# Optimization experiments

Hardware: AMD Instinct MI355X
Metric: run time of the kernel (lower is better)

Reference implementation:

```python
import jax, jax.numpy as jnp
import numpy as np

B, S, D, H, F = 2, 2048, 1024, 16, 4096
DH = D // H
EPS = 1e-6


def layer_norm(x, g, b):
    mu = jnp.mean(x, axis=-1, keepdims=True)
    var = jnp.mean(jnp.square(x - mu), axis=-1, keepdims=True)
    return (x - mu) * jax.lax.rsqrt(var + EPS) * g + b


def setup_inputs() -> dict:
    key = jax.random.key(0)
    ks = jax.random.split(key, 12)
    s_in = 1.0 / np.sqrt(D)
    s_ff = 1.0 / np.sqrt(F)
    return {
        "x_enc": jax.random.normal(ks[0], (B, S, D), jnp.float32),
        "x_pos": jax.random.normal(ks[1], (B, S, D), jnp.float32),
        "wq": jax.random.normal(ks[2], (D, D), jnp.float32) * s_in,
        "bq": jnp.zeros((D,), jnp.float32),
        "wk": jax.random.normal(ks[3], (D, D), jnp.float32) * s_in,
        "bk": jnp.zeros((D,), jnp.float32),
        "wv": jax.random.normal(ks[4], (D, D), jnp.float32) * s_in,
        "bv": jnp.zeros((D,), jnp.float32),
        "wc": jax.random.normal(ks[5], (D, D), jnp.float32) * s_in,
        "bc": jnp.zeros((D,), jnp.float32),
        "w1": jax.random.normal(ks[6], (D, F), jnp.float32) * s_in,
        "b1": jnp.zeros((F,), jnp.float32),
        "w2": jax.random.normal(ks[7], (F, D), jnp.float32) * s_ff,
        "b2": jnp.zeros((D,), jnp.float32),
        "g1": jnp.ones((D,), jnp.float32),
        "be1": jnp.zeros((D,), jnp.float32),
        "g2": jnp.ones((D,), jnp.float32),
        "be2": jnp.zeros((D,), jnp.float32),
    }


def reference(x_enc, x_pos, wq, bq, wk, bk, wv, bv, wc, bc, w1, b1, w2, b2, g1, be1, g2, be2):
    x = x_enc + x_pos  # [B,S,D]

    def split_heads(t):  # [B,S,D] -> [B,H,S,DH]
        return t.reshape(B, S, H, DH).transpose(0, 2, 1, 3)

    q = split_heads(x @ wq + bq)
    k = split_heads(x @ wk + bk)
    v = split_heads(x @ wv + bv)

    scale = jax.lax.rsqrt(jnp.asarray(DH, jnp.float32))
    logits = jnp.einsum("bhqd,bhkd->bhqk", q, k) * scale  # [B,H,S,S]
    weights = jax.nn.softmax(logits, axis=-1)
    attn = jnp.einsum("bhqk,bhkd->bhqd", weights, v)  # [B,H,S,DH]
    attn = attn.transpose(0, 2, 1, 3).reshape(B, S, D)
    attn = attn @ wc + bc

    # residual: x + LN(attn_out)   (dropout inactive in eval)
    a = x + layer_norm(attn, g1, be1)
    ffn = jnp.maximum(a @ w1 + b1, 0.0) @ w2 + b2
    out = a + layer_norm(ffn, g2, be2)
    return out
```

## Files before the change

### kernel.cpp

```cpp
#include <hip/hip_runtime.h>
#include <math.h>

#define B_ 2
#define S_ 2048
#define D_ 1024
#define H_ 16
#define F_ 4096

typedef __bf16 bf16_t;
typedef __bf16 bf16x8 __attribute__((ext_vector_type(8)));
typedef __bf16 bf16x4 __attribute__((ext_vector_type(4)));
typedef float f32x4 __attribute__((ext_vector_type(4)));
typedef float f32x16 __attribute__((ext_vector_type(16)));
typedef _Float16 f16x4 __attribute__((ext_vector_type(4)));
typedef _Float16 f16x8 __attribute__((ext_vector_type(8)));
typedef __fp16 h16x2 __attribute__((ext_vector_type(2)));

__device__ __forceinline__ bf16_t f2b(float f) { return (bf16_t)f; }

__device__ __forceinline__ void gld_lds16(const void* g, void* l) {
  __builtin_amdgcn_global_load_lds(
      (const __attribute__((address_space(1))) unsigned int*)g,
      (__attribute__((address_space(3))) unsigned int*)l, 16, 0, 0);
}

__device__ __forceinline__ void transpose_tile(const float* __restrict__ in,
                                               bf16_t* __restrict__ out,
                                               int K, int N, int bx, int by) {
  __shared__ float tile[64][65];
  int k0 = by * 64, n0 = bx * 64;
  int tid = threadIdx.x;
  int col4 = tid & 15;
  int row = tid >> 4;
#pragma unroll
  for (int rr = 0; rr < 4; ++rr) {
    int r = rr * 16 + row;
    float4 v = *reinterpret_cast<const float4*>(in + (size_t)(k0 + r) * N + n0 + col4 * 4);
    tile[r][col4 * 4 + 0] = v.x;
    tile[r][col4 * 4 + 1] = v.y;
    tile[r][col4 * 4 + 2] = v.z;
    tile[r][col4 * 4 + 3] = v.w;
  }
  __syncthreads();
#pragma unroll
  for (int rr = 0; rr < 4; ++rr) {
    int n = rr * 16 + row;
    bf16x4 o;
    o[0] = f2b(tile[col4 * 4 + 0][n]);
    o[1] = f2b(tile[col4 * 4 + 1][n]);
    o[2] = f2b(tile[col4 * 4 + 2][n]);
    o[3] = f2b(tile[col4 * 4 + 3][n]);
    *reinterpret_cast<bf16x4*>(out + (size_t)(n0 + n) * K + k0 + col4 * 4) = o;
  }
}

__global__ __launch_bounds__(256) void prep_kernel(
    const float* __restrict__ xe, const float* __restrict__ xp,
    bf16_t* __restrict__ XB,
    const float* __restrict__ wq, const float* __restrict__ wk,
    const float* __restrict__ wv, const float* __restrict__ wc,
    const float* __restrict__ w1, const float* __restrict__ w2,
    const float* __restrict__ bq, const float* __restrict__ bk,
    const float* __restrict__ bv,
    bf16_t* __restrict__ Wqkvt, bf16_t* __restrict__ wctb,
    bf16_t* __restrict__ w1tb, bf16_t* __restrict__ w2tb,
    float* __restrict__ bqkv) {
  int bid = blockIdx.x;
  if (bid < 4096) {
    int i = bid * 256 + threadIdx.x;
    float4 av = reinterpret_cast<const float4*>(xe)[i];
    float4 bv4 = reinterpret_cast<const float4*>(xp)[i];
    bf16x4 o;
    o[0] = f2b(av.x + bv4.x); o[1] = f2b(av.y + bv4.y);
    o[2] = f2b(av.z + bv4.z); o[3] = f2b(av.w + bv4.w);
    reinterpret_cast<bf16x4*>(XB)[i] = o;
    return;
  }
  int pb = bid - 4096;
  if (pb < 1024) {
    int seg = pb >> 8, local = pb & 255;
    const float* src = seg == 0 ? wq : (seg == 1 ? wk : (seg == 2 ? wv : wc));
    bf16_t* dst = seg == 3 ? wctb : Wqkvt + (size_t)seg * D_ * D_;
    transpose_tile(src, dst, D_, D_, local & 15, local >> 4);
  } else if (pb < 2048) {
    int local = pb - 1024;
    transpose_tile(w1, w1tb, D_, F_, local & 63, local >> 6);
  } else if (pb < 3072) {
    int local = pb - 2048;
    transpose_tile(w2, w2tb, F_, D_, local & 15, local >> 4);
  } else {
    int i = (pb - 3072) * 256 + threadIdx.x;
    const float* src = i < 1024 ? bq : (i < 2048 ? bk : bv);
    bqkv[i] = src[i & 1023];
  }
}

__global__ __launch_bounds__(256) void gemm_kernel(
    const bf16_t* __restrict__ A, const bf16_t* __restrict__ Bt,
    const float* __restrict__ bias,
    bf16_t* __restrict__ P0, bf16_t* __restrict__ P1,
    bf16_t* __restrict__ P2, bf16_t* __restrict__ P3,
    _Float16* __restrict__ VTout,
    int M, int N, int K, int relu, int kchunk, int rx, int ry) {
  __shared__ bf16_t As[128 * 64];
  __shared__ bf16_t Bs[128 * 64];
  int tid = threadIdx.x;
  int lane = tid & 63, wave = tid >> 6;
  int bx = blockIdx.x, by = blockIdx.y;
  if (rx) {
    int id = by * gridDim.x + bx;
    int j = id & 7, local = id >> 3;
    int regs_x = gridDim.x / rx;
    bx = (j % regs_x) * rx + local % rx;
    by = (j / regs_x) * ry + local / rx;
  }
  int bm = by * 128, bn = bx * 128;
  int wm = (wave >> 1) * 64, wn = (wave & 1) * 64;
  int m32 = lane & 31, khalf = lane >> 5;
  int z = blockIdx.z;
  int kbeg = z * kchunk, kend = kbeg + kchunk;
  f32x16 acc[2][2] = {};

  for (int kt = kbeg; kt < kend; kt += 64) {
    __syncthreads();
#pragma unroll
    for (int c = 0; c < 4; ++c) {
      int e = c * 256 + tid;
      int row = e >> 3, kg = e & 7;
      int kgs = kg ^ (row & 7);
      gld_lds16(A + (size_t)(bm + row) * K + kt + kgs * 8, As + e * 8);
    }
#pragma unroll
    for (int c = 0; c < 4; ++c) {
      int e = c * 256 + tid;
      int row = e >> 3, kg = e & 7;
      int kgs = kg ^ (row & 7);
      gld_lds16(Bt + (size_t)(bn + row) * K + kt + kgs * 8, Bs + e * 8);
    }
    __syncthreads();
#pragma unroll
    for (int kc = 0; kc < 4; ++kc) {
      bf16x8 af[2], bfr[2];
#pragma unroll
      for (int mi = 0; mi < 2; ++mi) {
        int row = wm + mi * 32 + m32;
        int kg = (kc * 2 + khalf) ^ (row & 7);
        af[mi] = *reinterpret_cast<const bf16x8*>(As + row * 64 + kg * 8);
      }
#pragma unroll
      for (int ni = 0; ni < 2; ++ni) {
        int row = wn + ni * 32 + m32;
        int kg = (kc * 2 + khalf) ^ (row & 7);
        bfr[ni] = *reinterpret_cast<const bf16x8*>(Bs + row * 64 + kg * 8);
      }
#pragma unroll
      for (int mi = 0; mi < 2; ++mi)
#pragma unroll
        for (int ni = 0; ni < 2; ++ni)
          acc[mi][ni] = __builtin_amdgcn_mfma_f32_32x32x16_bf16(af[mi], bfr[ni], acc[mi][ni], 0, 0, 0);
    }
  }
  bf16_t* Cb = z == 0 ? P0 : (z == 1 ? P1 : (z == 2 ? P2 : P3));
#pragma unroll
  for (int ni = 0; ni < 2; ++ni) {
    int n = bn + wn + ni * 32 + m32;
    float bz = (bias && z == 0) ? bias[n] : 0.f;
#pragma unroll
    for (int mi = 0; mi < 2; ++mi) {
      float vv[16];
#pragma unroll
      for (int r = 0; r < 16; ++r) {
        float v = acc[mi][ni][r] + bz;
        if (relu) v = fmaxf(v, 0.f);
        vv[r] = v;
      }
      if (VTout && n >= 2048) {
        int h = (n - 2048) >> 6, d = (n - 2048) & 63;
        int bb = bm >> 11;
        _Float16* vtr = VTout + ((size_t)((bb * H_ + h) * 64 + d)) * S_
                        + (bm & 2047) + wm + mi * 32;
#pragma unroll
        for (int g = 0; g < 4; ++g) {
          int off = ((2 * g + khalf) & 3) * 8 + (g >> 1) * 4;
          f16x4 hv;
          hv[0] = (_Float16)vv[g * 4 + 0]; hv[1] = (_Float16)vv[g * 4 + 1];
          hv[2] = (_Float16)vv[g * 4 + 2]; hv[3] = (_Float16)vv[g * 4 + 3];
          *reinterpret_cast<f16x4*>(vtr + off) = hv;
        }
      } else {
#pragma unroll
        for (int r = 0; r < 16; ++r) {
          int m = bm + wm + mi * 32 + (r & 3) + 8 * (r >> 2) + 4 * khalf;
          Cb[(size_t)m * N + n] = f2b(vv[r]);
        }
      }
    }
  }
}

__global__ __launch_bounds__(256) void attn_kernel(const bf16_t* __restrict__ Q,
                                                   const bf16_t* __restrict__ Kg,
                                                   const _Float16* __restrict__ VT,
                                                   bf16_t* __restrict__ O, int ldq) {
  __shared__ bf16_t Ks[128 * 64];
  __shared__ _Float16 Vs[64 * 128];
  int qt = blockIdx.x, h = blockIdx.y, b = blockIdx.z;
  int tid = threadIdx.x, wave = tid >> 6, lane = tid & 63;
  int qcol = lane & 15, grp = lane >> 4;
  int qbase = qt * 64 + wave * 16;
  const float kS = 0.125f * 1.4426950408889634f;
  const float kB = 12.0f * 1.4426950408889634f;
  const h16x2 one2 = {(__fp16)1.f, (__fp16)1.f};

  bf16x8 qf[2];
#pragma unroll
  for (int c = 0; c < 2; ++c)
    qf[c] = *reinterpret_cast<const bf16x8*>(
        Q + (size_t)(b * S_ + qbase + qcol) * ldq + h * 64 + c * 32 + grp * 8);
  const _Float16* vtb = VT + (size_t)((b * H_ + h) * 64) * S_;

  f32x4 oacc[4] = {};
  float lsum = 0.f;

  for (int t0 = 0; t0 < S_; t0 += 128) {
    __syncthreads();
#pragma unroll
    for (int cc = 0; cc < 4; ++cc) {
      int e = cc * 256 + tid;
      int row = e >> 3, kg = e & 7, kgs = kg ^ (row & 7);
      gld_lds16(Kg + (size_t)(b * S_ + t0 + row) * ldq + h * 64 + kgs * 8, Ks + e * 8);
    }
#pragma unroll
    for (int cc = 0; cc < 4; ++cc) {
      int e = cc * 256 + tid;
      int d = e >> 4, kc = e & 15, kcs = kc ^ (d & 7);
      gld_lds16(vtb + (size_t)d * S_ + t0 + kcs * 8, Vs + e * 8);
    }
    __syncthreads();
#pragma unroll
    for (int kb2 = 0; kb2 < 4; ++kb2) {
      f32x4 se = {}, so = {};
      int krowe = kb2 * 32 + qcol;
      int krowo = krowe + 16;
#pragma unroll
      for (int c = 0; c < 2; ++c) {
        int gce = (c * 4 + grp) ^ (krowe & 7);
        bf16x8 kfe = *reinterpret_cast<const bf16x8*>(Ks + krowe * 64 + gce * 8);
        se = __builtin_amdgcn_mfma_f32_16x16x32_bf16(kfe, qf[c], se, 0, 0, 0);
        int gco = (c * 4 + grp) ^ (krowo & 7);
        bf16x8 kfo = *reinterpret_cast<const bf16x8*>(Ks + krowo * 64 + gco * 8);
        so = __builtin_amdgcn_mfma_f32_16x16x32_bf16(kfo, qf[c], so, 0, 0, 0);
      }
      float pe0 = __builtin_amdgcn_exp2f(fmaf(se[0], kS, -kB));
      float pe1 = __builtin_amdgcn_exp2f(fmaf(se[1], kS, -kB));
      float pe2 = __builtin_amdgcn_exp2f(fmaf(se[2], kS, -kB));
      float pe3 = __builtin_amdgcn_exp2f(fmaf(se[3], kS, -kB));
      float po0 = __builtin_amdgcn_exp2f(fmaf(so[0], kS, -kB));
      float po1 = __builtin_amdgcn_exp2f(fmaf(so[1], kS, -kB));
      float po2 = __builtin_amdgcn_exp2f(fmaf(so[2], kS, -kB));
      float po3 = __builtin_amdgcn_exp2f(fmaf(so[3], kS, -kB));
      h16x2 e01 = __builtin_amdgcn_cvt_pkrtz(pe0, pe1);
      h16x2 e23 = __builtin_amdgcn_cvt_pkrtz(pe2, pe3);
      h16x2 q01 = __builtin_amdgcn_cvt_pkrtz(po0, po1);
      h16x2 q23 = __builtin_amdgcn_cvt_pkrtz(po2, po3);
      lsum = __builtin_amdgcn_fdot2(e01, one2, lsum, false);
      lsum = __builtin_amdgcn_fdot2(e23, one2, lsum, false);
      lsum = __builtin_amdgcn_fdot2(q01, one2, lsum, false);
      lsum = __builtin_amdgcn_fdot2(q23, one2, lsum, false);
      f16x8 pf;
      pf[0] = (_Float16)e01[0]; pf[1] = (_Float16)e01[1];
      pf[2] = (_Float16)e23[0]; pf[3] = (_Float16)e23[1];
      pf[4] = (_Float16)q01[0]; pf[5] = (_Float16)q01[1];
      pf[6] = (_Float16)q23[0]; pf[7] = (_Float16)q23[1];
#pragma unroll
      for (int db = 0; db < 4; ++db) {
        int d = db * 16 + qcol;
        int kc = (kb2 * 4 + grp) ^ (d & 7);
        f16x8 vf = *reinterpret_cast<const f16x8*>(Vs + d * 128 + kc * 8);
        oacc[db] = __builtin_amdgcn_mfma_f32_16x16x32_f16(vf, pf, oacc[db], 0, 0, 0);
      }
    }
  }

  lsum += __shfl_xor(lsum, 16, 64);
  lsum += __shfl_xor(lsum, 32, 64);
  float inv = 1.f / lsum;
  size_t rowbase = (size_t)(b * S_ + qbase + qcol) * D_ + h * 64;
#pragma unroll
  for (int db = 0; db < 4; ++db)
#pragma unroll
    for (int r = 0; r < 4; ++r)
      O[rowbase + db * 16 + grp * 4 + r] = f2b(oacc[db][r] * inv);
}

__global__ __launch_bounds__(256) void ln_res_kernel(const bf16_t* Y0,
                                                     const bf16_t* Y1,
                                                     const bf16_t* Y2,
                                                     const bf16_t* Y3,
                                                     int nY,
                                                     const bf16_t* Xres,
                                                     const float* __restrict__ g,
                                                     const float* __restrict__ be,
                                                     float* OutF,
                                                     bf16_t* OutB) {
  int row = blockIdx.x;
  int tid = threadIdx.x, wave = tid >> 6, lane = tid & 63;
  size_t base = (size_t)row * D_;
  bf16x4 y0 = reinterpret_cast<const bf16x4*>(Y0 + base)[tid];
  bf16x4 y1 = reinterpret_cast<const bf16x4*>(Y1 + base)[tid];
  float4 v;
  v.x = (float)y0[0] + (float)y1[0];
  v.y = (float)y0[1] + (float)y1[1];
  v.z = (float)y0[2] + (float)y1[2];
  v.w = (float)y0[3] + (float)y1[3];
  if (nY == 4) {
    bf16x4 y2 = reinterpret_cast<const bf16x4*>(Y2 + base)[tid];
    bf16x4 y3 = reinterpret_cast<const bf16x4*>(Y3 + base)[tid];
    v.x += (float)y2[0] + (float)y3[0];
    v.y += (float)y2[1] + (float)y3[1];
    v.z += (float)y2[2] + (float)y3[2];
    v.w += (float)y2[3] + (float)y3[3];
  }
  float s = v.x + v.y + v.z + v.w;
  float s2 = v.x * v.x + v.y * v.y + v.z * v.z + v.w * v.w;
#pragma unroll
  for (int off = 32; off > 0; off >>= 1) {
    s += __shfl_xor(s, off, 64);
    s2 += __shfl_xor(s2, off, 64);
  }
  __shared__ float red[2][4];
  if (lane == 0) { red[0][wave] = s; red[1][wave] = s2; }
  __syncthreads();
  s = red[0][0] + red[0][1] + red[0][2] + red[0][3];
  s2 = red[1][0] + red[1][1] + red[1][2] + red[1][3];
  float mu = s * (1.f / D_);
  float var = s2 * (1.f / D_) - mu * mu;
  float rstd = rsqrtf(var + 1e-6f);
  bf16x4 xr4 = reinterpret_cast<const bf16x4*>(Xres + base)[tid];
  float4 gv = reinterpret_cast<const float4*>(g)[tid];
  float4 bv = reinterpret_cast<const float4*>(be)[tid];
  float4 o;
  o.x = (float)xr4[0] + (v.x - mu) * rstd * gv.x + bv.x;
  o.y = (float)xr4[1] + (v.y - mu) * rstd * gv.y + bv.y;
  o.z = (float)xr4[2] + (v.z - mu) * rstd * gv.z + bv.z;
  o.w = (float)xr4[3] + (v.w - mu) * rstd * gv.w + bv.w;
  if (OutF) reinterpret_cast<float4*>(OutF + base)[tid] = o;
  if (OutB) {
    bf16x4 ob; ob[0] = f2b(o.x); ob[1] = f2b(o.y); ob[2] = f2b(o.z); ob[3] = f2b(o.w);
    reinterpret_cast<bf16x4*>(OutB + base)[tid] = ob;
  }
}

extern "C" void kernel_launch(void* const* d_in, const int* in_sizes, int n_in,
                              void* d_out, int out_size, void* d_ws, size_t ws_size,
                              hipStream_t stream) {
  const float* x_enc = (const float*)d_in[0];
  const float* x_pos = (const float*)d_in[1];
  const float* wq = (const float*)d_in[2];
  const float* bq = (const float*)d_in[3];
  const float* wk = (const float*)d_in[4];
  const float* bk = (const float*)d_in[5];
  const float* wv = (const float*)d_in[6];
  const float* bv = (const float*)d_in[7];
  const float* wc = (const float*)d_in[8];
  const float* bc = (const float*)d_in[9];
  const float* w1 = (const float*)d_in[10];
  const float* b1 = (const float*)d_in[11];
  const float* w2 = (const float*)d_in[12];
  const float* b2 = (const float*)d_in[13];
  const float* g1 = (const float*)d_in[14];
  const float* be1 = (const float*)d_in[15];
  const float* g2 = (const float*)d_in[16];
  const float* be2 = (const float*)d_in[17];

  const size_t MB = 1024ull * 1024ull;
  char* w = (char*)d_ws;
  bf16_t* F0 = (bf16_t*)(w + 0);
  bf16_t* F1p = (bf16_t*)(w + 8 * MB);
  bf16_t* Wqkvt = (bf16_t*)(w + 32 * MB);
  bf16_t* wctb = (bf16_t*)(w + 38 * MB);
  bf16_t* w1tb = (bf16_t*)(w + 40 * MB);
  bf16_t* w2tb = (bf16_t*)(w + 48 * MB);
  bf16_t* XB = (bf16_t*)(w + 56 * MB);
  bf16_t* QKVB = (bf16_t*)(w + 64 * MB);
  bf16_t* Pp0 = (bf16_t*)(w + 64 * MB);
  bf16_t* Pp1 = (bf16_t*)(w + 72 * MB);
  bf16_t* F2 = (bf16_t*)(w + 64 * MB);
  bf16_t* F3 = (bf16_t*)(w + 72 * MB);
  bf16_t* ATTNB = (bf16_t*)(w + 88 * MB);
  float* bqkv = (float*)(w + 96 * MB);
  _Float16* VTg = (_Float16*)(w + 104 * MB);
  bf16_t* F1B = (bf16_t*)(w + 112 * MB);

  const int rows = B_ * S_;

  prep_kernel<<<7180, 256, 0, stream>>>(x_enc, x_pos, XB,
                                        wq, wk, wv, wc, w1, w2, bq, bk, bv,
                                        Wqkvt, wctb, w1tb, w2tb, bqkv);

  gemm_kernel<<<dim3(3 * D_ / 128, rows / 128, 1), 256, 0, stream>>>(
      XB, Wqkvt, bqkv, QKVB, nullptr, nullptr, nullptr, VTg,
      rows, 3 * D_, D_, 0, D_, 12, 8);

  attn_kernel<<<dim3(S_ / 64, H_, B_), 256, 0, stream>>>(
      QKVB, QKVB + D_, VTg, ATTNB, 3 * D_);

  gemm_kernel<<<dim3(D_ / 128, rows / 128, 2), 256, 0, stream>>>(
      ATTNB, wctb, bc, Pp0, Pp1, nullptr, nullptr, nullptr,
      rows, D_, D_, 0, D_ / 2, 8, 4);

  ln_res_kernel<<<rows, 256, 0, stream>>>(Pp0, Pp1, Pp0, Pp0, 2, XB, g1, be1,
                                          nullptr, XB);

  gemm_kernel<<<dim3(F_ / 128, rows / 128, 1), 256, 0, stream>>>(
      XB, w1tb, b1, F1B, nullptr, nullptr, nullptr, nullptr,
      rows, F_, D_, 1, D_, 16, 8);

  gemm_kernel<<<dim3(D_ / 128, rows / 128, 4), 256, 0, stream>>>(
      F1B, w2tb, b2, F0, F1p, F2, F3, nullptr,
      rows, D_, F_, 0, F_ / 4, 8, 4);

  ln_res_kernel<<<rows, 256, 0, stream>>>(F0, F1p, F2, F3, 4, XB, g2, be2,
                                          (float*)d_out, nullptr);
}
```

Baseline: 377.7 us.

## Rewrite GEMM as 256x256 tile, 8-wave kernel with double-buffered phased LDS pipeline

The GEMM tile grows from 128x128 with 4 waves to 256x256 with 8 waves. The K loop becomes a software pipeline of eight phases over double-buffered LDS halves, with async global-to-LDS loads overlapping MFMA work, explicit vmcnt/lgkmcnt waits, and setprio around the MFMA bursts. The output-projection GEMM moves to 4-way split-K to keep enough blocks, and the LN kernel now sums four partials. The aim is more data reuse per tile and latency hiding, at the cost of fewer blocks (low occupancy on small GEMMs), 128KB of LDS, and hand-tuned synchronisation that is fragile.

```diff
diff --git a/kernel.cpp b/kernel.cpp
--- a/kernel.cpp
+++ b/kernel.cpp
@@ -95,15 +95,65 @@
   }
 }
 
-__global__ __launch_bounds__(256) void gemm_kernel(
+
+__device__ __forceinline__ void stage_half(const bf16_t* __restrict__ G,
+                                           int grow0, int K, int kt,
+                                           bf16_t* lb, int tid) {
+#pragma unroll
+  for (int c = 0; c < 2; ++c) {
+    int e = c * 512 + tid;
+    int rl = e >> 3, kg = e & 7;
+    int kgs = kg ^ (rl & 7);
+    gld_lds16(G + (size_t)(grow0 + rl) * K + kt + kgs * 8, lb + e * 8);
+  }
+}
+
+template <int DBUF, int MH, int NH, int SARR, int SBUF, int SH, int DOWAIT>
+__device__ __forceinline__ void gemm_phase(
+    bf16_t* As, bf16_t* Bs, const bf16_t* __restrict__ A,
+    const bf16_t* __restrict__ Bt, f32x16 (&acc)[4][2], int bm, int bn, int K,
+    int kbeg, int stile, int tid, int m32, int khalf, int ra0, int ra1, int rb) {
+  const bf16_t* abase = As + (DBUF * 2 + MH) * 8192;
+  const bf16_t* bbase = Bs + (DBUF * 2 + NH) * 8192;
+  bf16x8 af0[4], af1[4], bfx[4];
+#pragma unroll
+  for (int kc = 0; kc < 4; ++kc) {
+    int kg = ((kc * 2 + khalf) ^ (m32 & 7)) * 8;
+    af0[kc] = *reinterpret_cast<const bf16x8*>(abase + ra0 * 64 + kg);
+    af1[kc] = *reinterpret_cast<const bf16x8*>(abase + ra1 * 64 + kg);
+    bfx[kc] = *reinterpret_cast<const bf16x8*>(bbase + rb * 64 + kg);
+  }
+  {
+    const bf16_t* G = SARR ? Bt : A;
+    int g0 = (SARR ? bn : bm) + SH * 128;
+    bf16_t* lb = (SARR ? Bs : As) + (SBUF * 2 + SH) * 8192;
+    stage_half(G, g0, K, kbeg + stile * 64, lb, tid);
+  }
+  if (DOWAIT) asm volatile("s_waitcnt vmcnt(4)" ::: "memory");
+  __builtin_amdgcn_s_barrier();
+  asm volatile("s_waitcnt lgkmcnt(0)" ::: "memory");
+  __builtin_amdgcn_sched_barrier(0);
+  __builtin_amdgcn_s_setprio(1);
+#pragma unroll
+  for (int kc = 0; kc < 4; ++kc) {
+    acc[MH * 2 + 0][NH] = __builtin_amdgcn_mfma_f32_32x32x16_bf16(
+        af0[kc], bfx[kc], acc[MH * 2 + 0][NH], 0, 0, 0);
+    acc[MH * 2 + 1][NH] = __builtin_amdgcn_mfma_f32_32x32x16_bf16(
+        af1[kc], bfx[kc], acc[MH * 2 + 1][NH], 0, 0, 0);
+  }
+  __builtin_amdgcn_s_setprio(0);
+  __builtin_amdgcn_s_barrier();
+}
+
+__global__ __launch_bounds__(512) void gemm_kernel(
     const bf16_t* __restrict__ A, const bf16_t* __restrict__ Bt,
     const float* __restrict__ bias,
     bf16_t* __restrict__ P0, bf16_t* __restrict__ P1,
     bf16_t* __restrict__ P2, bf16_t* __restrict__ P3,
     _Float16* __restrict__ VTout,
     int M, int N, int K, int relu, int kchunk, int rx, int ry) {
-  __shared__ bf16_t As[128 * 64];
-  __shared__ bf16_t Bs[128 * 64];
+  __shared__ bf16_t As[4 * 8192];
+  __shared__ bf16_t Bs[4 * 8192];
   int tid = threadIdx.x;
   int lane = tid & 63, wave = tid >> 6;
   int bx = blockIdx.x, by = blockIdx.y;
@@ -114,59 +164,46 @@
     bx = (j % regs_x) * rx + local % rx;
     by = (j / regs_x) * ry + local / rx;
   }
-  int bm = by * 128, bn = bx * 128;
-  int wm = (wave >> 1) * 64, wn = (wave & 1) * 64;
+  int bm = by * 256, bn = bx * 256;
+  int wm = wave >> 2, wn = wave & 3;
   int m32 = lane & 31, khalf = lane >> 5;
+  int ra0 = wm * 64 + m32, ra1 = ra0 + 32, rb = wn * 32 + m32;
   int z = blockIdx.z;
-  int kbeg = z * kchunk, kend = kbeg + kchunk;
-  f32x16 acc[2][2] = {};
-
-  for (int kt = kbeg; kt < kend; kt += 64) {
-    __syncthreads();
-#pragma unroll
-    for (int c = 0; c < 4; ++c) {
-      int e = c * 256 + tid;
-      int row = e >> 3, kg = e & 7;
-      int kgs = kg ^ (row & 7);
-      gld_lds16(A + (size_t)(bm + row) * K + kt + kgs * 8, As + e * 8);
-    }
-#pragma unroll
-    for (int c = 0; c < 4; ++c) {
-      int e = c * 256 + tid;
-      int row = e >> 3, kg = e & 7;
-      int kgs = kg ^ (row & 7);
-      gld_lds16(Bt + (size_t)(bn + row) * K + kt + kgs * 8, Bs + e * 8);
-    }
-    __syncthreads();
-#pragma unroll
-    for (int kc = 0; kc < 4; ++kc) {
-      bf16x8 af[2], bfr[2];
-#pragma unroll
-      for (int mi = 0; mi < 2; ++mi) {
-        int row = wm + mi * 32 + m32;
-        int kg = (kc * 2 + khalf) ^ (row & 7);
-        af[mi] = *reinterpret_cast<const bf16x8*>(As + row * 64 + kg * 8);
-      }
-#pragma unroll
-      for (int ni = 0; ni < 2; ++ni) {
-        int row = wn + ni * 32 + m32;
-        int kg = (kc * 2 + khalf) ^ (row & 7);
-        bfr[ni] = *reinterpret_cast<const bf16x8*>(Bs + row * 64 + kg * 8);
-      }
-#pragma unroll
-      for (int mi = 0; mi < 2; ++mi)
-#pragma unroll
-        for (int ni = 0; ni < 2; ++ni)
-          acc[mi][ni] = __builtin_amdgcn_mfma_f32_32x32x16_bf16(af[mi], bfr[ni], acc[mi][ni], 0, 0, 0);
-    }
-  }
+  int kbeg = z * kchunk;
+  int nt = kchunk >> 6, ntm1 = nt - 1;
+  f32x16 acc[4][2] = {};
+
+  stage_half(A, bm, K, kbeg, As + 0 * 8192, tid);
+  stage_half(Bt, bn, K, kbeg, Bs + 0 * 8192, tid);
+  stage_half(A, bm + 128, K, kbeg, As + 1 * 8192, tid);
+  stage_half(Bt, bn + 128, K, kbeg, Bs + 1 * 8192, tid);
+  stage_half(A, bm, K, kbeg + 64, As + 2 * 8192, tid);
+  stage_half(Bt, bn, K, kbeg + 64, Bs + 2 * 8192, tid);
+  asm volatile("s_waitcnt vmcnt(4)" ::: "memory");
+  __builtin_amdgcn_s_barrier();
+
+  int nt2 = nt >> 1;
+  for (int j = 0; j < nt2; ++j) {
+    int t1 = 2 * j + 1;
+    int t2 = 2 * j + 2 > ntm1 ? ntm1 : 2 * j + 2;
+    int t3 = 2 * j + 3 > ntm1 ? ntm1 : 2 * j + 3;
+    gemm_phase<0, 0, 0, 0, 1, 1, 0>(As, Bs, A, Bt, acc, bm, bn, K, kbeg, t1, tid, m32, khalf, ra0, ra1, rb);
+    gemm_phase<0, 0, 1, 1, 1, 1, 0>(As, Bs, A, Bt, acc, bm, bn, K, kbeg, t1, tid, m32, khalf, ra0, ra1, rb);
+    gemm_phase<0, 1, 0, 0, 0, 0, 0>(As, Bs, A, Bt, acc, bm, bn, K, kbeg, t2, tid, m32, khalf, ra0, ra1, rb);
+    gemm_phase<0, 1, 1, 1, 0, 0, 1>(As, Bs, A, Bt, acc, bm, bn, K, kbeg, t2, tid, m32, khalf, ra0, ra1, rb);
+    gemm_phase<1, 0, 0, 0, 0, 1, 0>(As, Bs, A, Bt, acc, bm, bn, K, kbeg, t2, tid, m32, khalf, ra0, ra1, rb);
+    gemm_phase<1, 0, 1, 1, 0, 1, 0>(As, Bs, A, Bt, acc, bm, bn, K, kbeg, t2, tid, m32, khalf, ra0, ra1, rb);
+    gemm_phase<1, 1, 0, 0, 1, 0, 0>(As, Bs, A, Bt, acc, bm, bn, K, kbeg, t3, tid, m32, khalf, ra0, ra1, rb);
+    gemm_phase<1, 1, 1, 1, 1, 0, 1>(As, Bs, A, Bt, acc, bm, bn, K, kbeg, t3, tid, m32, khalf, ra0, ra1, rb);
+  }
+
   bf16_t* Cb = z == 0 ? P0 : (z == 1 ? P1 : (z == 2 ? P2 : P3));
 #pragma unroll
   for (int ni = 0; ni < 2; ++ni) {
-    int n = bn + wn + ni * 32 + m32;
+    int n = bn + ni * 128 + wn * 32 + m32;
     float bz = (bias && z == 0) ? bias[n] : 0.f;
 #pragma unroll
-    for (int mi = 0; mi < 2; ++mi) {
+    for (int mi = 0; mi < 4; ++mi) {
       float vv[16];
 #pragma unroll
       for (int r = 0; r < 16; ++r) {
@@ -174,11 +211,11 @@
         if (relu) v = fmaxf(v, 0.f);
         vv[r] = v;
       }
+      int sb = bm + (mi >> 1) * 128 + wm * 64 + (mi & 1) * 32;
       if (VTout && n >= 2048) {
         int h = (n - 2048) >> 6, d = (n - 2048) & 63;
-        int bb = bm >> 11;
-        _Float16* vtr = VTout + ((size_t)((bb * H_ + h) * 64 + d)) * S_
-                        + (bm & 2047) + wm + mi * 32;
+        int bb = sb >> 11;
+        _Float16* vtr = VTout + ((size_t)((bb * H_ + h) * 64 + d)) * S_ + (sb & 2047);
 #pragma unroll
         for (int g = 0; g < 4; ++g) {
           int off = ((2 * g + khalf) & 3) * 8 + (g >> 1) * 4;
@@ -190,7 +227,7 @@
       } else {
 #pragma unroll
         for (int r = 0; r < 16; ++r) {
-          int m = bm + wm + mi * 32 + (r & 3) + 8 * (r >> 2) + 4 * khalf;
+          int m = sb + (r & 3) + 8 * (r >> 2) + 4 * khalf;
           Cb[(size_t)m * N + n] = f2b(vv[r]);
         }
       }
@@ -385,11 +422,13 @@
   bf16_t* QKVB = (bf16_t*)(w + 64 * MB);
   bf16_t* Pp0 = (bf16_t*)(w + 64 * MB);
   bf16_t* Pp1 = (bf16_t*)(w + 72 * MB);
+  bf16_t* Pp2 = (bf16_t*)(w + 80 * MB);
   bf16_t* F2 = (bf16_t*)(w + 64 * MB);
   bf16_t* F3 = (bf16_t*)(w + 72 * MB);
   bf16_t* ATTNB = (bf16_t*)(w + 88 * MB);
   float* bqkv = (float*)(w + 96 * MB);
   _Float16* VTg = (_Float16*)(w + 104 * MB);
+  bf16_t* Pp3 = (bf16_t*)(w + 104 * MB);
   bf16_t* F1B = (bf16_t*)(w + 112 * MB);
 
   const int rows = B_ * S_;
@@ -398,27 +437,27 @@
                                         wq, wk, wv, wc, w1, w2, bq, bk, bv,
                                         Wqkvt, wctb, w1tb, w2tb, bqkv);
 
-  gemm_kernel<<<dim3(3 * D_ / 128, rows / 128, 1), 256, 0, stream>>>(
+  gemm_kernel<<<dim3(3 * D_ / 256, rows / 256, 1), 512, 0, stream>>>(
       XB, Wqkvt, bqkv, QKVB, nullptr, nullptr, nullptr, VTg,
-      rows, 3 * D_, D_, 0, D_, 12, 8);
+      rows, 3 * D_, D_, 0, D_, 3, 8);
 
   attn_kernel<<<dim3(S_ / 64, H_, B_), 256, 0, stream>>>(
       QKVB, QKVB + D_, VTg, ATTNB, 3 * D_);
 
-  gemm_kernel<<<dim3(D_ / 128, rows / 128, 2), 256, 0, stream>>>(
-      ATTNB, wctb, bc, Pp0, Pp1, nullptr, nullptr, nullptr,
-      rows, D_, D_, 0, D_ / 2, 8, 4);
-
-  ln_res_kernel<<<rows, 256, 0, stream>>>(Pp0, Pp1, Pp0, Pp0, 2, XB, g1, be1,
+  gemm_kernel<<<dim3(D_ / 256, rows / 256, 4), 512, 0, stream>>>(
+      ATTNB, wctb, bc, Pp0, Pp1, Pp2, Pp3, nullptr,
+      rows, D_, D_, 0, D_ / 4, 2, 4);
+
+  ln_res_kernel<<<rows, 256, 0, stream>>>(Pp0, Pp1, Pp2, Pp3, 4, XB, g1, be1,
                                           nullptr, XB);
 
-  gemm_kernel<<<dim3(F_ / 128, rows / 128, 1), 256, 0, stream>>>(
+  gemm_kernel<<<dim3(F_ / 256, rows / 256, 1), 512, 0, stream>>>(
       XB, w1tb, b1, F1B, nullptr, nullptr, nullptr, nullptr,
-      rows, F_, D_, 1, D_, 16, 8);
-
-  gemm_kernel<<<dim3(D_ / 128, rows / 128, 4), 256, 0, stream>>>(
+      rows, F_, D_, 1, D_, 4, 8);
+
+  gemm_kernel<<<dim3(D_ / 256, rows / 256, 4), 512, 0, stream>>>(
       F1B, w2tb, b2, F0, F1p, F2, F3, nullptr,
-      rows, D_, F_, 0, F_ / 4, 8, 4);
+      rows, D_, F_, 0, F_ / 4, 2, 4);
 
   ln_res_kernel<<<rows, 256, 0, stream>>>(F0, F1p, F2, F3, 4, XB, g2, be2,
                                           (float*)d_out, nullptr);
```

New measurement: 374.5 us. Within noise of the previous version (-0.9%).
